# Optimization experiments

Measured on AMD Instinct MI355X. Metric: run time of the kernel, lower is better.

## Reference

```python
import jax, jax.numpy as jnp
import numpy as np

B, LQ, LK, E, H, NF, NE, HID = 4, 8192, 8192, 256, 8, 2, 4, 256


def _split(x, h):
    b, l, e = x.shape
    return x.reshape(b, l, h, e // h).transpose(0, 2, 1, 3)  # (B,H,L,D)


def _merge(x):
    b, h, l, d = x.shape
    return x.transpose(0, 2, 1, 3).reshape(b, l, h * d)


def _experts(x, W1, b1, W2, b2, W3, b3):
    # x: (B,N,in); W*: (E, out, in). Returns (E,B,N,out). Exact (erf) GELU as torch.
    h = jax.nn.gelu(jnp.einsum('bni,ehi->ebnh', x, W1) + b1[:, None, None, :], approximate=False)
    h = jax.nn.gelu(jnp.einsum('ebnh,egh->ebng', h, W2) + b2[:, None, None, :], approximate=False)
    return jnp.einsum('ebng,eog->ebno', h, W3) + b3[:, None, None, :]


def _combine(expert_out, scores):
    # expert_out: (E,B,N,out); scores: (B,N,1,E) -> (B,N,out)
    return jnp.einsum('ebno,bne->bno', expert_out, scores[:, :, 0, :])


def _forward(scores, query, input_functions,
             ca_Wq, ca_bq, ca_Wk, ca_bk, ca_Wv, ca_bv, ca_Wo, ca_bo,
             sa_Wq, sa_bq, sa_Wk, sa_bk, sa_Wv, sa_bv, sa_Wo, sa_bo,
             f1_W1, f1_b1, f1_W2, f1_b2, f1_W3, f1_b3,
             f2_W1, f2_b1, f2_W2, f2_b2, f2_W3, f2_b3):
    h = H
    # ---- cross attention over NF input functions ----
    q = jax.nn.softmax(_split(query @ ca_Wq.T + ca_bq, h), -1)  # (B,H,Lq,D)
    k = jnp.einsum('fble,fde->fbld', input_functions, ca_Wk) + ca_bk[:, None, None, :]
    v = jnp.einsum('fble,fde->fbld', input_functions, ca_Wv) + ca_bv[:, None, None, :]
    f, b, lk, e = k.shape
    d = e // h
    k = jax.nn.softmax(k.reshape(f, b, lk, h, d).transpose(0, 1, 3, 2, 4), -1)  # (F,B,H,Lk,D)
    v = v.reshape(f, b, lk, h, d).transpose(0, 1, 3, 2, 4)
    k_sum = k.sum(3, keepdims=True)                       # (F,B,H,1,D)
    alpha = 1.0 / (q[None] * k_sum).sum(-1, keepdims=True)  # (F,B,H,Lq,1)
    tmp = jnp.einsum('fbhld,fbhlv->fbhdv', k, v)          # (F,B,H,D,D)
    out = (alpha * jnp.einsum('bhld,fbhdv->fbhlv', q, tmp)).mean(0)  # (B,H,Lq,D)
    ca = (_merge(q) + _merge(out)) @ ca_Wo.T + ca_bo
    # expert FFN1 + score-weighted combine, residual
    query = query + _combine(_experts(ca, f1_W1, f1_b1, f1_W2, f1_b2, f1_W3, f1_b3), scores)
    # ---- self attention ----
    q2 = jax.nn.softmax(_split(query @ sa_Wq.T + sa_bq, h), -1)
    k2 = jax.nn.softmax(_split(query @ sa_Wk.T + sa_bk, h), -1)
    v2 = _split(query @ sa_Wv.T + sa_bv, h)
    k_sum2 = k2.sum(2, keepdims=True)
    alpha2 = 1.0 / (q2 * k_sum2).sum(-1, keepdims=True)
    tmp2 = jnp.einsum('bhld,bhlv->bhdv', k2, v2)
    out2 = alpha2 * jnp.einsum('bhld,bhdv->bhlv', q2, tmp2)
    sa = (_merge(q2) + _merge(out2)) @ sa_Wo.T + sa_bo
    query = query + _combine(_experts(sa, f2_W1, f2_b1, f2_W2, f2_b2, f2_W3, f2_b3), scores)
    return query


def setup_inputs() -> dict:
    ks = iter(jax.random.split(jax.random.key(0), 64))
    def p(shape):
        return jax.random.normal(next(ks), shape, jnp.float32) * 0.02
    inp = {
        'scores': jax.random.uniform(next(ks), (B, LQ, 1, NE), jnp.float32),
        'query': jax.random.normal(next(ks), (B, LQ, E), jnp.float32),
        'input_functions': jax.random.normal(next(ks), (NF, B, LK, E), jnp.float32),
        'ca_Wq': p((E, E)), 'ca_bq': p((E,)),
        'ca_Wk': p((NF, E, E)), 'ca_bk': p((NF, E)),
        'ca_Wv': p((NF, E, E)), 'ca_bv': p((NF, E)),
        'ca_Wo': p((E, E)), 'ca_bo': p((E,)),
        'sa_Wq': p((E, E)), 'sa_bq': p((E,)),
        'sa_Wk': p((E, E)), 'sa_bk': p((E,)),
        'sa_Wv': p((E, E)), 'sa_bv': p((E,)),
        'sa_Wo': p((E, E)), 'sa_bo': p((E,)),
        'f1_W1': p((NE, HID, E)), 'f1_b1': p((NE, HID)),
        'f1_W2': p((NE, HID, HID)), 'f1_b2': p((NE, HID)),
        'f1_W3': p((NE, HID, HID)), 'f1_b3': p((NE, HID)),
        'f2_W1': p((NE, HID, E)), 'f2_b1': p((NE, HID)),
        'f2_W2': p((NE, HID, HID)), 'f2_b2': p((NE, HID)),
        'f2_W3': p((NE, HID, HID)), 'f2_b3': p((NE, HID)),
    }
    return inp


def reference(scores, query, input_functions,
              ca_Wq, ca_bq, ca_Wk, ca_bk, ca_Wv, ca_bv, ca_Wo, ca_bo,
              sa_Wq, sa_bq, sa_Wk, sa_bk, sa_Wv, sa_bv, sa_Wo, sa_bo,
              f1_W1, f1_b1, f1_W2, f1_b2, f1_W3, f1_b3,
              f2_W1, f2_b1, f2_W2, f2_b2, f2_W3, f2_b3):
    return _forward(scores, query, input_functions,
                    ca_Wq, ca_bq, ca_Wk, ca_bk, ca_Wv, ca_bv, ca_Wo, ca_bo,
                    sa_Wq, sa_bq, sa_Wk, sa_bk, sa_Wv, sa_bv, sa_Wo, sa_bo,
                    f1_W1, f1_b1, f1_W2, f1_b2, f1_W3, f1_b3,
                    f2_W1, f2_b1, f2_W2, f2_b2, f2_W3, f2_b3)
```

## Files before the change

### kernel.cpp

```cpp
#include <hip/hip_runtime.h>


typedef unsigned short u16;
typedef __attribute__((ext_vector_type(8))) short   bs8;
typedef __attribute__((ext_vector_type(4))) float   f32x4;
typedef __attribute__((ext_vector_type(16))) float  f32x16;

__device__ __forceinline__ float bf2f(u16 u) {
  union { float f; unsigned i; } c; c.i = ((unsigned)u) << 16; return c.f;
}
__device__ __forceinline__ u16 f2bf(float f) {
  union { float f; unsigned i; } c; c.f = f;
  unsigned x = c.i;
  return (u16)((x + 0x7fffu + ((x >> 16) & 1u)) >> 16);
}
__device__ __forceinline__ unsigned pack2(float a, float b) {
  return (unsigned)f2bf(a) | ((unsigned)f2bf(b) << 16);
}
__device__ __forceinline__ float gelu_f(float x) {
  const float t = x * (0.7978845608f + 0.0356774081f * x * x);
  return x * __builtin_amdgcn_rcpf(1.f + __expf(-2.f * t));
}

#define EPI_PLAIN 0
#define EPI_QSM   4

template <bool AF32, int EPI>
__global__ __launch_bounds__(256, 4) void gemm256(
    const void* __restrict__ Ain, const u16* __restrict__ W,
    const float* __restrict__ bias, u16* __restrict__ outb) {
  __shared__ int4 ash[512];
  __shared__ int4 wsh[1024];
  const int tid = threadIdx.x;
  const int m0 = blockIdx.x * 64, n0 = blockIdx.y * 128;
  const int wave = tid >> 6, lane = tid & 63;
  const int wm = (wave >> 1) * 32, wn = (wave & 1) * 64;
  const int lr = lane & 15, lk = lane >> 4;
  f32x4 acc[2][4];
#pragma unroll
  for (int m = 0; m < 2; ++m)
#pragma unroll
    for (int n = 0; n < 4; ++n) acc[m][n] = f32x4{0.f, 0.f, 0.f, 0.f};

  const float* Af = (const float*)Ain;
  const u16*   Ab = (const u16*)Ain;

  for (int kt = 0; kt < 4; ++kt) {
    const int k0 = kt * 64;
    if (kt) __syncthreads();
#pragma unroll
    for (int it = 0; it < 2; ++it) {
      const int s = tid + it * 256;
      const int row = s >> 3, c16 = s & 7;
      const int dst = (row << 3) | (c16 ^ (row & 7));
      const long src = (long)(m0 + row) * 256 + k0 + c16 * 8;
      int4 val;
      if constexpr (AF32) {
        const float4* p = (const float4*)(Af + src);
        const float4 x = p[0], y = p[1];
        val.x = pack2(x.x, x.y); val.y = pack2(x.z, x.w);
        val.z = pack2(y.x, y.y); val.w = pack2(y.z, y.w);
      } else {
        val = *(const int4*)(Ab + src);
      }
      ash[dst] = val;
    }
#pragma unroll
    for (int it = 0; it < 4; ++it) {
      const int s = tid + it * 256;
      const int row = s >> 3, c16 = s & 7;
      const int dst = (row << 3) | (c16 ^ (row & 7));
      wsh[dst] = *(const int4*)(W + (long)(n0 + row) * 256 + k0 + c16 * 8);
    }
    __syncthreads();
#pragma unroll
    for (int kk = 0; kk < 2; ++kk) {
      bs8 af[2], wf[4];
#pragma unroll
      for (int m = 0; m < 2; ++m) {
        const int row = wm + m * 16 + lr;
        af[m] = *(const bs8*)&ash[(row << 3) | ((kk * 4 + lk) ^ (row & 7))];
      }
#pragma unroll
      for (int n = 0; n < 4; ++n) {
        const int row = wn + n * 16 + lr;
        wf[n] = *(const bs8*)&wsh[(row << 3) | ((kk * 4 + lk) ^ (row & 7))];
      }
#pragma unroll
      for (int m = 0; m < 2; ++m)
#pragma unroll
        for (int n = 0; n < 4; ++n)
          acc[m][n] = __builtin_amdgcn_mfma_f32_16x16x32_bf16(af[m], wf[n],
                                                              acc[m][n], 0, 0, 0);
    }
  }
  if constexpr (EPI == EPI_QSM) {
#pragma unroll
    for (int m = 0; m < 2; ++m) {
      const int rb = m0 + wm + m * 16 + lk * 4;
#pragma unroll
      for (int j = 0; j < 4; ++j) {
#pragma unroll
        for (int hh = 0; hh < 2; ++hh) {
          const int c0 = n0 + wn + (2 * hh) * 16 + lr;
          const float p0 = __expf(acc[m][2 * hh][j] + bias[c0]);
          const float p1 = __expf(acc[m][2 * hh + 1][j] + bias[c0 + 16]);
          float s = p0 + p1;
#pragma unroll
          for (int o = 8; o >= 1; o >>= 1) s += __shfl_xor(s, o);
          const float inv = 1.0f / s;
          outb[(long)(rb + j) * 256 + c0]      = f2bf(p0 * inv);
          outb[(long)(rb + j) * 256 + c0 + 16] = f2bf(p1 * inv);
        }
      }
    }
  } else {
#pragma unroll
    for (int m = 0; m < 2; ++m) {
      const int rb = m0 + wm + m * 16 + lk * 4;
#pragma unroll
      for (int n = 0; n < 4; ++n) {
        const int gc = n0 + wn + n * 16 + lr;
        const float bv = bias[gc];
#pragma unroll
        for (int j = 0; j < 4; ++j)
          outb[(long)(rb + j) * 256 + gc] = f2bf(acc[m][n][j] + bv);
      }
    }
  }
}

__global__ __launch_bounds__(1024, 4) void ffn4(
    const u16* __restrict__ X, const u16* __restrict__ WX, int wbase,
    const float* __restrict__ b1, const float* __restrict__ b2,
    const float* __restrict__ b3, const float* __restrict__ scores,
    const float* __restrict__ csrc, float* __restrict__ outf) {
  __shared__ int4 xsh[2048];
  __shared__ int4 hsh[2048];
  const int tid = threadIdx.x, wave = tid >> 6, lane = tid & 63;
  const int wm = (wave >> 3) * 32;
  const int wn8 = wave & 7;
  const int lr = lane & 15, lk = lane >> 4;
  const long m0 = (long)blockIdx.x * 64;

#pragma unroll
  for (int it = 0; it < 2; ++it) {
    const int s = tid + it * 1024;
    const int row = s >> 5, c8 = s & 31;
    const int cs = (c8 & 24) | ((c8 ^ row) & 7);
    xsh[row * 32 + cs] = *(const int4*)(X + (m0 + row) * 256 + c8 * 8);
  }
  __syncthreads();

  f32x4 oacc[2][2];
#pragma unroll
  for (int m = 0; m < 2; ++m)
#pragma unroll
    for (int n = 0; n < 2; ++n) oacc[m][n] = f32x4{0.f, 0.f, 0.f, 0.f};
  f32x4 acc[2][2];

  for (int e = 0; e < 4; ++e) {
#pragma unroll 1
    for (int l = 0; l < 3; ++l) {
      const u16* wp = WX + (long)(wbase + l * 4 + e) * 65536 + (long)lane * 8;
      const int4* asrc = (l == 0) ? xsh : hsh;
#pragma unroll
      for (int m = 0; m < 2; ++m)
#pragma unroll
        for (int n = 0; n < 2; ++n) acc[m][n] = f32x4{0.f, 0.f, 0.f, 0.f};
#pragma unroll
      for (int kt = 0; kt < 8; ++kt) {
        bs8 af[2], wf[2];
        const int c8 = kt * 4 + lk;
#pragma unroll
        for (int m = 0; m < 2; ++m) {
          const int row = wm + m * 16 + lr;
          const int cs = (c8 & 24) | ((c8 ^ row) & 7);
          af[m] = *(const bs8*)&asrc[row * 32 + cs];
        }
#pragma unroll
        for (int n = 0; n < 2; ++n)
          wf[n] = *(const bs8*)(wp + ((kt * 16 + wn8 * 2 + n) << 9));
        __builtin_amdgcn_s_setprio(1);
#pragma unroll
        for (int m = 0; m < 2; ++m)
#pragma unroll
          for (int n = 0; n < 2; ++n)
            acc[m][n] = __builtin_amdgcn_mfma_f32_16x16x32_bf16(
                af[m], wf[n], acc[m][n], 0, 0, 0);
        __builtin_amdgcn_s_setprio(0);
      }
      if (l < 2) {
        __syncthreads();
        const float* bb = (l == 0 ? b1 : b2) + e * 256;
        u16* hp = (u16*)hsh;
#pragma unroll
        for (int m = 0; m < 2; ++m)
#pragma unroll
          for (int n = 0; n < 2; ++n) {
            const int col = wn8 * 32 + n * 16 + lr;
            const float bv = bb[col];
            const int c8w = col >> 3;
#pragma unroll
            for (int j = 0; j < 4; ++j) {
              const int row = wm + m * 16 + lk * 4 + j;
              const int cs = (c8w & 24) | ((c8w ^ row) & 7);
              hp[row * 256 + cs * 8 + (col & 7)] =
                  f2bf(gelu_f(acc[m][n][j] + bv));
            }
          }
        __syncthreads();
      } else {
#pragma unroll
        for (int m = 0; m < 2; ++m) {
#pragma unroll
          for (int j = 0; j < 4; ++j) {
            const float sc = scores[(m0 + wm + m * 16 + lk * 4 + j) * 4 + e];
#pragma unroll
            for (int n = 0; n < 2; ++n)
              oacc[m][n][j] +=
                  sc * (acc[m][n][j] + b3[e * 256 + wn8 * 32 + n * 16 + lr]);
          }
        }
      }
    }
  }
#pragma unroll
  for (int m = 0; m < 2; ++m) {
#pragma unroll
    for (int n = 0; n < 2; ++n) {
      const int col = wn8 * 32 + n * 16 + lr;
#pragma unroll
      for (int j = 0; j < 4; ++j) {
        const long idx = (m0 + wm + m * 16 + lk * 4 + j) * 256 + col;
        outf[idx] = csrc[idx] + oacc[m][n][j];
      }
    }
  }
}

__global__ __launch_bounds__(1024, 4) void kvstats(
    const float* __restrict__ A0, const float* __restrict__ A1,
    const u16* __restrict__ Wk0, const u16* __restrict__ Wk1,
    const u16* __restrict__ Wv0, const u16* __restrict__ Wv1,
    const float* __restrict__ bk0, const float* __restrict__ bk1,
    const float* __restrict__ bv0, const float* __restrict__ bv1,
    float* __restrict__ pks, float* __restrict__ ptm) {
  __shared__ __align__(16) char smem[73728];
  int4* ash  = (int4*)smem;
  int4* wksh = ash + 512;
  int4* wvsh = wksh + 2048;
  u16* KnT = (u16*)smem;
  u16* VT  = KnT + 256 * 72;
  const int tid = threadIdx.x;
  const int wave = tid >> 6, lane = tid & 63;
  const int lr = lane & 15, lk = lane >> 4;
  const int kvsel = wave >> 3, w3 = wave & 7;
  const int wm = (w3 >> 2) * 32, wn = (w3 & 3) * 64;
  const int fb = blockIdx.y, ch = blockIdx.x;
  const int f = fb >> 2, b = fb & 3;
  const float* Ain = f ? A1 : A0;
  const u16* Wk = f ? Wk1 : Wk0;
  const u16* Wv = f ? Wv1 : Wv0;
  const float* bk = f ? bk1 : bk0;
  const float* bv = f ? bv1 : bv0;
  const long r0 = (long)b * 8192 + (long)ch * 64;

  f32x4 acc[2][4];
#pragma unroll
  for (int m = 0; m < 2; ++m)
#pragma unroll
    for (int n = 0; n < 4; ++n) acc[m][n] = f32x4{0.f, 0.f, 0.f, 0.f};

  for (int kt = 0; kt < 4; ++kt) {
    const int k0 = kt * 64;
    if (kt) __syncthreads();
    if (tid < 512) {
      const int row = tid >> 3, c16 = tid & 7;
      const int dst = (row << 3) | (c16 ^ (row & 7));
      const float4* p = (const float4*)(Ain + (r0 + row) * 256 + k0 + c16 * 8);
      const float4 x = p[0], y = p[1];
      int4 val;
      val.x = pack2(x.x, x.y); val.y = pack2(x.z, x.w);
      val.z = pack2(y.x, y.y); val.w = pack2(y.z, y.w);
      ash[dst] = val;
    }
#pragma unroll
    for (int it = 0; it < 2; ++it) {
      const int s = tid + it * 1024;
      const int row = s >> 3, c16 = s & 7;
      const int dst = (row << 3) | (c16 ^ (row & 7));
      wksh[dst] = *(const int4*)(Wk + (long)row * 256 + k0 + c16 * 8);
      wvsh[dst] = *(const int4*)(Wv + (long)row * 256 + k0 + c16 * 8);
    }
    __syncthreads();
    const int4* wsh = kvsel ? wvsh : wksh;
#pragma unroll
    for (int kk = 0; kk < 2; ++kk) {
      bs8 af[2], wf[4];
#pragma unroll
      for (int m = 0; m < 2; ++m) {
        const int row = wm + m * 16 + lr;
        af[m] = *(const bs8*)&ash[(row << 3) | ((kk * 4 + lk) ^ (row & 7))];
      }
#pragma unroll
      for (int n = 0; n < 4; ++n) {
        const int row = wn + n * 16 + lr;
        wf[n] = *(const bs8*)&wsh[(row << 3) | ((kk * 4 + lk) ^ (row & 7))];
      }
#pragma unroll
      for (int m = 0; m < 2; ++m)
#pragma unroll
        for (int n = 0; n < 4; ++n)
          acc[m][n] = __builtin_amdgcn_mfma_f32_16x16x32_bf16(af[m], wf[n],
                                                              acc[m][n], 0, 0, 0);
    }
  }
  __syncthreads();

  const float* bias = kvsel ? bv : bk;
  if (kvsel == 0) {
#pragma unroll
    for (int m = 0; m < 2; ++m)
#pragma unroll
      for (int j = 0; j < 4; ++j)
#pragma unroll
        for (int hh = 0; hh < 2; ++hh) {
          const int c0 = wn + (2 * hh) * 16 + lr;
          const float p0 = __expf(acc[m][2 * hh][j] + bias[c0]);
          const float p1 = __expf(acc[m][2 * hh + 1][j] + bias[c0 + 16]);
          float s = p0 + p1;
#pragma unroll
          for (int o = 8; o >= 1; o >>= 1) s += __shfl_xor(s, o);
          const float inv = 1.0f / s;
          acc[m][2 * hh][j] = p0 * inv;
          acc[m][2 * hh + 1][j] = p1 * inv;
        }
  }
  {
    u16* T = kvsel ? VT : KnT;
#pragma unroll
    for (int m = 0; m < 2; ++m) {
      const int rb = wm + m * 16 + lk * 4;
#pragma unroll
      for (int n = 0; n < 4; ++n) {
        const int col = wn + n * 16 + lr;
        float v0 = acc[m][n][0], v1 = acc[m][n][1];
        float v2 = acc[m][n][2], v3 = acc[m][n][3];
        if (kvsel) {
          const float bb = bias[col];
          v0 += bb; v1 += bb; v2 += bb; v3 += bb;
        }
        uint2 w;
        w.x = pack2(v0, v1); w.y = pack2(v2, v3);
        *(uint2*)(T + col * 72 + rb) = w;
      }
    }
  }
  __syncthreads();

  if (kvsel == 0) {
    const int h = w3;
    f32x16 aT, aK;
#pragma unroll
    for (int r = 0; r < 16; ++r) { aT[r] = 0.f; aK[r] = 0.f; }
    bs8 ones;
#pragma unroll
    for (int e = 0; e < 8; ++e) ones[e] = (short)0x3F80;
    const u16* kcol = KnT + (h * 32 + (lane & 31)) * 72;
    const u16* vcol = VT  + (h * 32 + (lane & 31)) * 72;
    const int hi8 = (lane >> 5) * 8;
#pragma unroll
    for (int ks = 0; ks < 4; ++ks) {
      const bs8 a  = *(const bs8*)(kcol + ks * 16 + hi8);
      const bs8 vb = *(const bs8*)(vcol + ks * 16 + hi8);
      aT = __builtin_amdgcn_mfma_f32_32x32x16_bf16(vb, a, aT, 0, 0, 0);
      aK = __builtin_amdgcn_mfma_f32_32x32x16_bf16(a, ones, aK, 0, 0, 0);
    }
    const long blk = (long)fb * gridDim.x + ch;
    float* po = ptm + blk * 8192 + h * 1024;
#pragma unroll
    for (int r = 0; r < 16; ++r) {
      const int dv = (r & 3) + 8 * (r >> 2) + 4 * (lane >> 5);
      po[dv * 32 + (lane & 31)] = aT[r];
    }
    if ((lane & 31) == 0) {
#pragma unroll
      for (int r = 0; r < 16; ++r) {
        const int dk = (r & 3) + 8 * (r >> 2) + 4 * (lane >> 5);
        pks[blk * 256 + h * 32 + dk] = aK[r];
      }
    }
  }
}

__global__ void reduceStats(const float* __restrict__ pk,
                            const float* __restrict__ pt,
                            float* __restrict__ ksum, float* __restrict__ tmp) {
  const int b = blockIdx.y;
  const int i = blockIdx.x * 256 + threadIdx.x;
  float s = 0.f;
  if (i < 256) {
    const float* p = pk + (long)b * 128 * 256 + i;
    for (int c = 0; c < 128; ++c) s += p[c * 256];
    ksum[(long)b * 256 + i] = s;
  } else {
    const int j = i - 256;
    const float* p = pt + (long)b * 128 * 8192 + j;
    for (int c = 0; c < 128; ++c) s += p[c * 8192];
    tmp[(long)b * 8192 + j] = s;
  }
}

template <int F>
__global__ __launch_bounds__(256, 2) void mixk(const u16* __restrict__ q,
                                               const float* __restrict__ ksum,
                                               const float* __restrict__ tmp,
                                               u16* __restrict__ out) {
  constexpr int LF = (F == 2) ? 1 : 0;
  constexpr int QS = 264;
  __shared__ u16 qsh[64 * QS];
  __shared__ float alsh[64][17];
  __shared__ float ksh[8][F * 36];
  const int t = threadIdx.x;
  const int h = t >> 5, dv = t & 31;
  const int b = blockIdx.y;
  const long row0 = (long)b * 8192 + (long)blockIdx.x * 64;

#pragma unroll
  for (int it = 0; it < 8; ++it) {
    const int i = t + it * 256;
    const int r = i >> 5, c = i & 31;
    *(int4*)&qsh[r * QS + c * 8] = *(const int4*)&q[(row0 + r) * 256 + c * 8];
  }
#pragma unroll
  for (int f = 0; f < F; ++f)
    ksh[h][f * 36 + dv] = ksum[((long)f * 4 + b) * 256 + t];
  float tr[F][32];
#pragma unroll
  for (int f = 0; f < F; ++f) {
    const float* tp = tmp + ((long)f * 4 + b) * 8192 + h * 1024 + dv * 32;
#pragma unroll
    for (int c = 0; c < 8; ++c) {
      const float4 v = *(const float4*)(tp + c * 4);
      tr[f][c * 4] = v.x; tr[f][c * 4 + 1] = v.y;
      tr[f][c * 4 + 2] = v.z; tr[f][c * 4 + 3] = v.w;
    }
  }
  __syncthreads();

  for (int d = t; d < 64 * 8 * F; d += 256) {
    const int f = d & (F - 1);
    const int hh = (d >> LF) & 7;
    const int r = d >> (3 + LF);
    const u16* qp = &qsh[r * QS + hh * 32];
    const float* kp = &ksh[hh][f * 36];
    float s = 0.f;
#pragma unroll
    for (int c = 0; c < 4; ++c) {
      const bs8 qa = *(const bs8*)(qp + c * 8);
#pragma unroll
      for (int j = 0; j < 8; ++j) s += bf2f((u16)qa[j]) * kp[c * 8 + j];
    }
    alsh[r][(hh << LF) | f] = 1.0f / s;
  }
  __syncthreads();

#pragma unroll 2
  for (int r = 0; r < 64; ++r) {
    float qr[32];
    const u16* qp = &qsh[r * QS + h * 32];
#pragma unroll
    for (int c = 0; c < 4; ++c) {
      const bs8 qa = *(const bs8*)(qp + c * 8);
#pragma unroll
      for (int j = 0; j < 8; ++j) qr[c * 8 + j] = bf2f((u16)qa[j]);
    }
    float acc = 0.f;
#pragma unroll
    for (int f = 0; f < F; ++f) {
      float s0 = 0.f, s1 = 0.f;
#pragma unroll
      for (int dk = 0; dk < 32; dk += 2) {
        s0 += qr[dk] * tr[f][dk];
        s1 += qr[dk + 1] * tr[f][dk + 1];
      }
      acc += (s0 + s1) * alsh[r][(h << LF) | f];
    }
    const float qv = bf2f(qsh[r * QS + t]);
    out[(row0 + r) * 256 + t] = f2bf(qv + acc * (1.0f / (float)F));
  }
}

struct WTab10 { const float* p[10]; };
__global__ void convW(WTab10 tab, u16* __restrict__ dst) {
  const int s = blockIdx.y;
  const long i = ((long)blockIdx.x * 256 + threadIdx.x) * 4;
  const float4 v = *(const float4*)(tab.p[s] + i);
  ushort4 o;
  o.x = f2bf(v.x); o.y = f2bf(v.y); o.z = f2bf(v.z); o.w = f2bf(v.w);
  *(ushort4*)(dst + (long)s * 65536 + i) = o;
}

struct WTab24 { const float* p[24]; };
__global__ void convWX(WTab24 tab, u16* __restrict__ dst) {
  const int s = blockIdx.y;
  const int o8 = blockIdx.x * 256 + threadIdx.x;
  const int kt = o8 >> 10, nt = (o8 >> 6) & 15, lane = o8 & 63;
  const int row = nt * 16 + (lane & 15);
  const int col = kt * 32 + (lane >> 4) * 8;
  const float* src = tab.p[s] + row * 256 + col;
  const float4 a = *(const float4*)src;
  const float4 b = *(const float4*)(src + 4);
  int4 val;
  val.x = pack2(a.x, a.y); val.y = pack2(a.z, a.w);
  val.z = pack2(b.x, b.y); val.w = pack2(b.z, b.w);
  *(int4*)(dst + (long)s * 65536 + (long)o8 * 8) = val;
}

extern "C" void kernel_launch(void* const* d_in, const int* in_sizes, int n_in,
                              void* d_out, int out_size, void* d_ws, size_t ws_size,
                              hipStream_t stream) {
  (void)in_sizes; (void)n_in; (void)out_size; (void)ws_size;
  const float* scores = (const float*)d_in[0];
  const float* query  = (const float*)d_in[1];
  const float* IF     = (const float*)d_in[2];
  const float* ca_Wq = (const float*)d_in[3];  const float* ca_bq = (const float*)d_in[4];
  const float* ca_Wk = (const float*)d_in[5];  const float* ca_bk = (const float*)d_in[6];
  const float* ca_Wv = (const float*)d_in[7];  const float* ca_bv = (const float*)d_in[8];
  const float* ca_Wo = (const float*)d_in[9];  const float* ca_bo = (const float*)d_in[10];
  const float* sa_Wq = (const float*)d_in[11]; const float* sa_bq = (const float*)d_in[12];
  const float* sa_Wk = (const float*)d_in[13]; const float* sa_bk = (const float*)d_in[14];
  const float* sa_Wv = (const float*)d_in[15]; const float* sa_bv = (const float*)d_in[16];
  const float* sa_Wo = (const float*)d_in[17]; const float* sa_bo = (const float*)d_in[18];
  const float* f1W1 = (const float*)d_in[19]; const float* f1b1 = (const float*)d_in[20];
  const float* f1W2 = (const float*)d_in[21]; const float* f1b2 = (const float*)d_in[22];
  const float* f1W3 = (const float*)d_in[23]; const float* f1b3 = (const float*)d_in[24];
  const float* f2W1 = (const float*)d_in[25]; const float* f2b1 = (const float*)d_in[26];
  const float* f2W2 = (const float*)d_in[27]; const float* f2b2 = (const float*)d_in[28];
  const float* f2W3 = (const float*)d_in[29]; const float* f2b3 = (const float*)d_in[30];

  char* ws = (char*)d_ws;
  u16* X0 = (u16*)(ws);
  u16* X1 = (u16*)(ws + 16777216);
  u16* X2 = (u16*)(ws + 33554432);
  float* ptmBig = (float*)(ws + 16777216);
  u16* W16 = (u16*)(ws + 67108864);
  u16* WX  = (u16*)(ws + 68419584);
  float* ksum = (float*)(ws + 71565312);
  float* tmpb = (float*)(ws + 71573504);
  float* pks  = (float*)(ws + 71835648);
  float* qacc = (float*)d_out;

  WTab10 tab;
  tab.p[0] = ca_Wq; tab.p[1] = ca_Wk; tab.p[2] = ca_Wk + 65536;
  tab.p[3] = ca_Wv; tab.p[4] = ca_Wv + 65536; tab.p[5] = ca_Wo;
  tab.p[6] = sa_Wq; tab.p[7] = sa_Wk; tab.p[8] = sa_Wv; tab.p[9] = sa_Wo;
  convW<<<dim3(64, 10), 256, 0, stream>>>(tab, W16);

  WTab24 tabx;
  for (int e = 0; e < 4; ++e) {
    tabx.p[0 + e]  = f1W1 + e * 65536;
    tabx.p[4 + e]  = f1W2 + e * 65536;
    tabx.p[8 + e]  = f1W3 + e * 65536;
    tabx.p[12 + e] = f2W1 + e * 65536;
    tabx.p[16 + e] = f2W2 + e * 65536;
    tabx.p[20 + e] = f2W3 + e * 65536;
  }
  convWX<<<dim3(32, 24), 256, 0, stream>>>(tabx, WX);

  const dim3 gg(512, 2), gb(256);
  gemm256<true, EPI_QSM><<<gg, gb, 0, stream>>>(query, W16 + 0 * 65536L, ca_bq, X0);
  kvstats<<<dim3(128, 8), 1024, 0, stream>>>(
      IF, IF + 8388608L,
      W16 + 1 * 65536L, W16 + 2 * 65536L, W16 + 3 * 65536L, W16 + 4 * 65536L,
      ca_bk, ca_bk + 256, ca_bv, ca_bv + 256, pks, ptmBig);
  reduceStats<<<dim3(33, 8), 256, 0, stream>>>(pks, ptmBig, ksum, tmpb);
  mixk<2><<<dim3(128, 4), 256, 0, stream>>>(X0, ksum, tmpb, X1);
  gemm256<false, EPI_PLAIN><<<gg, gb, 0, stream>>>(X1, W16 + 5 * 65536L, ca_bo, X2);
  ffn4<<<512, 1024, 0, stream>>>(X2, WX, 0, f1b1, f1b2, f1b3, scores, query, qacc);
  gemm256<true, EPI_QSM><<<gg, gb, 0, stream>>>(qacc, W16 + 6 * 65536L, sa_bq, X0);
  kvstats<<<dim3(128, 4), 1024, 0, stream>>>(
      qacc, qacc,
      W16 + 7 * 65536L, W16 + 7 * 65536L, W16 + 8 * 65536L, W16 + 8 * 65536L,
      sa_bk, sa_bk, sa_bv, sa_bv, pks, ptmBig);
  reduceStats<<<dim3(33, 4), 256, 0, stream>>>(pks, ptmBig, ksum, tmpb);
  mixk<1><<<dim3(128, 4), 256, 0, stream>>>(X0, ksum, tmpb, X1);
  gemm256<false, EPI_PLAIN><<<gg, gb, 0, stream>>>(X1, W16 + 9 * 65536L, sa_bo, X2);
  ffn4<<<512, 1024, 0, stream>>>(X2, WX, 12, f2b1, f2b2, f2b3, scores, qacc, qacc);
}
```

Baseline: 415.1 us.

## Fuse output projection into expert FFN kernel and repartition waves by column

The attention output projection (Wo GEMM plus bias) now runs inside ffn4 as a prologue, so the separate gemm256 launch and the X2 round trip through global memory are dropped. ffn4's wave layout changes from a 2x8 grid of 32x32 tiles to 16 waves that each own a 16-column strip across all 64 rows. Each weight fragment is loaded once per k-step and reused by four MFMAs, and the next fragment is prefetched in software. The weight repack layout is reordered to match, with two extra slots for the Wo matrices, and the workspace offsets shift accordingly. In exchange, each block does an extra 256x256 GEMM, and A-fragment LDS reads per wave double.

```diff
diff --git a/kernel.cpp b/kernel.cpp
--- a/kernel.cpp
+++ b/kernel.cpp
@@ -131,16 +131,17 @@
 }
 
 __global__ __launch_bounds__(1024, 4) void ffn4(
-    const u16* __restrict__ X, const u16* __restrict__ WX, int wbase,
+    const u16* __restrict__ Xin, const u16* __restrict__ WX,
+    int wPslot, int wbase, const float* __restrict__ bP,
     const float* __restrict__ b1, const float* __restrict__ b2,
     const float* __restrict__ b3, const float* __restrict__ scores,
     const float* __restrict__ csrc, float* __restrict__ outf) {
   __shared__ int4 xsh[2048];
   __shared__ int4 hsh[2048];
   const int tid = threadIdx.x, wave = tid >> 6, lane = tid & 63;
-  const int wm = (wave >> 3) * 32;
-  const int wn8 = wave & 7;
+  const int ng = wave;
   const int lr = lane & 15, lk = lane >> 4;
+  const int col = ng * 16 + lr;
   const long m0 = (long)blockIdx.x * 64;
 
 #pragma unroll
@@ -148,93 +149,119 @@
     const int s = tid + it * 1024;
     const int row = s >> 5, c8 = s & 31;
     const int cs = (c8 & 24) | ((c8 ^ row) & 7);
-    xsh[row * 32 + cs] = *(const int4*)(X + (m0 + row) * 256 + c8 * 8);
+    hsh[row * 32 + cs] = *(const int4*)(Xin + (m0 + row) * 256 + c8 * 8);
   }
   __syncthreads();
 
-  f32x4 oacc[2][2];
-#pragma unroll
-  for (int m = 0; m < 2; ++m)
-#pragma unroll
-    for (int n = 0; n < 2; ++n) oacc[m][n] = f32x4{0.f, 0.f, 0.f, 0.f};
-  f32x4 acc[2][2];
+  f32x4 acc[4];
+
+  {
+    const u16* wp = WX + (((long)wPslot) << 16) + (ng << 12) + lane * 8;
+#pragma unroll
+    for (int m = 0; m < 4; ++m) acc[m] = f32x4{0.f, 0.f, 0.f, 0.f};
+    bs8 wf, wfn;
+    wf = *(const bs8*)(wp);
+#pragma unroll
+    for (int kt = 0; kt < 8; ++kt) {
+      if (kt < 7) wfn = *(const bs8*)(wp + (kt + 1) * 512);
+      bs8 af[4];
+      const int c8 = kt * 4 + lk;
+#pragma unroll
+      for (int m = 0; m < 4; ++m) {
+        const int row = m * 16 + lr;
+        const int cs = (c8 & 24) | ((c8 ^ row) & 7);
+        af[m] = *(const bs8*)&hsh[row * 32 + cs];
+      }
+      __builtin_amdgcn_s_setprio(1);
+#pragma unroll
+      for (int m = 0; m < 4; ++m)
+        acc[m] = __builtin_amdgcn_mfma_f32_16x16x32_bf16(af[m], wf, acc[m],
+                                                         0, 0, 0);
+      __builtin_amdgcn_s_setprio(0);
+      wf = wfn;
+    }
+    __syncthreads();
+    const float bv = bP[col];
+    u16* xp = (u16*)xsh;
+    const int c8w = col >> 3;
+#pragma unroll
+    for (int m = 0; m < 4; ++m)
+#pragma unroll
+      for (int j = 0; j < 4; ++j) {
+        const int row = m * 16 + lk * 4 + j;
+        const int cs = (c8w & 24) | ((c8w ^ row) & 7);
+        xp[row * 256 + cs * 8 + (col & 7)] = f2bf(acc[m][j] + bv);
+      }
+    __syncthreads();
+  }
+
+  f32x4 oacc[4];
+#pragma unroll
+  for (int m = 0; m < 4; ++m) oacc[m] = f32x4{0.f, 0.f, 0.f, 0.f};
 
   for (int e = 0; e < 4; ++e) {
 #pragma unroll 1
     for (int l = 0; l < 3; ++l) {
-      const u16* wp = WX + (long)(wbase + l * 4 + e) * 65536 + (long)lane * 8;
+      const u16* wp = WX + (((long)(wbase + l * 4 + e)) << 16) +
+                      (ng << 12) + lane * 8;
       const int4* asrc = (l == 0) ? xsh : hsh;
 #pragma unroll
-      for (int m = 0; m < 2; ++m)
-#pragma unroll
-        for (int n = 0; n < 2; ++n) acc[m][n] = f32x4{0.f, 0.f, 0.f, 0.f};
+      for (int m = 0; m < 4; ++m) acc[m] = f32x4{0.f, 0.f, 0.f, 0.f};
+      bs8 wf, wfn;
+      wf = *(const bs8*)(wp);
 #pragma unroll
       for (int kt = 0; kt < 8; ++kt) {
-        bs8 af[2], wf[2];
+        if (kt < 7) wfn = *(const bs8*)(wp + (kt + 1) * 512);
+        bs8 af[4];
         const int c8 = kt * 4 + lk;
 #pragma unroll
-        for (int m = 0; m < 2; ++m) {
-          const int row = wm + m * 16 + lr;
+        for (int m = 0; m < 4; ++m) {
+          const int row = m * 16 + lr;
           const int cs = (c8 & 24) | ((c8 ^ row) & 7);
           af[m] = *(const bs8*)&asrc[row * 32 + cs];
         }
-#pragma unroll
-        for (int n = 0; n < 2; ++n)
-          wf[n] = *(const bs8*)(wp + ((kt * 16 + wn8 * 2 + n) << 9));
         __builtin_amdgcn_s_setprio(1);
 #pragma unroll
-        for (int m = 0; m < 2; ++m)
-#pragma unroll
-          for (int n = 0; n < 2; ++n)
-            acc[m][n] = __builtin_amdgcn_mfma_f32_16x16x32_bf16(
-                af[m], wf[n], acc[m][n], 0, 0, 0);
+        for (int m = 0; m < 4; ++m)
+          acc[m] = __builtin_amdgcn_mfma_f32_16x16x32_bf16(af[m], wf, acc[m],
+                                                           0, 0, 0);
         __builtin_amdgcn_s_setprio(0);
+        wf = wfn;
       }
       if (l < 2) {
         __syncthreads();
-        const float* bb = (l == 0 ? b1 : b2) + e * 256;
+        const float bv = (l == 0 ? b1 : b2)[e * 256 + col];
         u16* hp = (u16*)hsh;
-#pragma unroll
-        for (int m = 0; m < 2; ++m)
-#pragma unroll
-          for (int n = 0; n < 2; ++n) {
-            const int col = wn8 * 32 + n * 16 + lr;
-            const float bv = bb[col];
-            const int c8w = col >> 3;
-#pragma unroll
-            for (int j = 0; j < 4; ++j) {
-              const int row = wm + m * 16 + lk * 4 + j;
-              const int cs = (c8w & 24) | ((c8w ^ row) & 7);
-              hp[row * 256 + cs * 8 + (col & 7)] =
-                  f2bf(gelu_f(acc[m][n][j] + bv));
-            }
+        const int c8w = col >> 3;
+#pragma unroll
+        for (int m = 0; m < 4; ++m)
+#pragma unroll
+          for (int j = 0; j < 4; ++j) {
+            const int row = m * 16 + lk * 4 + j;
+            const int cs = (c8w & 24) | ((c8w ^ row) & 7);
+            hp[row * 256 + cs * 8 + (col & 7)] =
+                f2bf(gelu_f(acc[m][j] + bv));
           }
         __syncthreads();
       } else {
-#pragma unroll
-        for (int m = 0; m < 2; ++m) {
+        const float b3v = b3[e * 256 + col];
+#pragma unroll
+        for (int m = 0; m < 4; ++m) {
 #pragma unroll
           for (int j = 0; j < 4; ++j) {
-            const float sc = scores[(m0 + wm + m * 16 + lk * 4 + j) * 4 + e];
-#pragma unroll
-            for (int n = 0; n < 2; ++n)
-              oacc[m][n][j] +=
-                  sc * (acc[m][n][j] + b3[e * 256 + wn8 * 32 + n * 16 + lr]);
+            const float sc = scores[(m0 + m * 16 + lk * 4 + j) * 4 + e];
+            oacc[m][j] += sc * (acc[m][j] + b3v);
           }
         }
       }
     }
   }
 #pragma unroll
-  for (int m = 0; m < 2; ++m) {
-#pragma unroll
-    for (int n = 0; n < 2; ++n) {
-      const int col = wn8 * 32 + n * 16 + lr;
-#pragma unroll
-      for (int j = 0; j < 4; ++j) {
-        const long idx = (m0 + wm + m * 16 + lk * 4 + j) * 256 + col;
-        outf[idx] = csrc[idx] + oacc[m][n][j];
-      }
+  for (int m = 0; m < 4; ++m) {
+#pragma unroll
+    for (int j = 0; j < 4; ++j) {
+      const long idx = (m0 + m * 16 + lk * 4 + j) * 256 + col;
+      outf[idx] = csrc[idx] + oacc[m][j];
     }
   }
 }
@@ -502,12 +529,14 @@
   *(ushort4*)(dst + (long)s * 65536 + i) = o;
 }
 
-struct WTab24 { const float* p[24]; };
-__global__ void convWX(WTab24 tab, u16* __restrict__ dst) {
+struct WTab26 { const float* p[26]; };
+__global__ void convWX(WTab26 tab, u16* __restrict__ dst) {
   const int s = blockIdx.y;
   const int o8 = blockIdx.x * 256 + threadIdx.x;
-  const int kt = o8 >> 10, nt = (o8 >> 6) & 15, lane = o8 & 63;
-  const int row = nt * 16 + (lane & 15);
+  const int lane = o8 & 63;
+  const int kt = (o8 >> 6) & 7;
+  const int ng = o8 >> 9;
+  const int row = ng * 16 + (lane & 15);
   const int col = kt * 32 + (lane >> 4) * 8;
   const float* src = tab.p[s] + row * 256 + col;
   const float4 a = *(const float4*)src;
@@ -543,13 +572,12 @@
   char* ws = (char*)d_ws;
   u16* X0 = (u16*)(ws);
   u16* X1 = (u16*)(ws + 16777216);
-  u16* X2 = (u16*)(ws + 33554432);
   float* ptmBig = (float*)(ws + 16777216);
   u16* W16 = (u16*)(ws + 67108864);
   u16* WX  = (u16*)(ws + 68419584);
-  float* ksum = (float*)(ws + 71565312);
-  float* tmpb = (float*)(ws + 71573504);
-  float* pks  = (float*)(ws + 71835648);
+  float* ksum = (float*)(ws + 71827456);
+  float* tmpb = (float*)(ws + 71835648);
+  float* pks  = (float*)(ws + 72097792);
   float* qacc = (float*)d_out;
 
   WTab10 tab;
@@ -558,7 +586,7 @@
   tab.p[6] = sa_Wq; tab.p[7] = sa_Wk; tab.p[8] = sa_Wv; tab.p[9] = sa_Wo;
   convW<<<dim3(64, 10), 256, 0, stream>>>(tab, W16);
 
-  WTab24 tabx;
+  WTab26 tabx;
   for (int e = 0; e < 4; ++e) {
     tabx.p[0 + e]  = f1W1 + e * 65536;
     tabx.p[4 + e]  = f1W2 + e * 65536;
@@ -567,7 +595,9 @@
     tabx.p[16 + e] = f2W2 + e * 65536;
     tabx.p[20 + e] = f2W3 + e * 65536;
   }
-  convWX<<<dim3(32, 24), 256, 0, stream>>>(tabx, WX);
+  tabx.p[24] = ca_Wo;
+  tabx.p[25] = sa_Wo;
+  convWX<<<dim3(32, 26), 256, 0, stream>>>(tabx, WX);
 
   const dim3 gg(512, 2), gb(256);
   gemm256<true, EPI_QSM><<<gg, gb, 0, stream>>>(query, W16 + 0 * 65536L, ca_bq, X0);
@@ -577,8 +607,8 @@
       ca_bk, ca_bk + 256, ca_bv, ca_bv + 256, pks, ptmBig);
   reduceStats<<<dim3(33, 8), 256, 0, stream>>>(pks, ptmBig, ksum, tmpb);
   mixk<2><<<dim3(128, 4), 256, 0, stream>>>(X0, ksum, tmpb, X1);
-  gemm256<false, EPI_PLAIN><<<gg, gb, 0, stream>>>(X1, W16 + 5 * 65536L, ca_bo, X2);
-  ffn4<<<512, 1024, 0, stream>>>(X2, WX, 0, f1b1, f1b2, f1b3, scores, query, qacc);
+  ffn4<<<512, 1024, 0, stream>>>(X1, WX, 24, 0, ca_bo,
+                                 f1b1, f1b2, f1b3, scores, query, qacc);
   gemm256<true, EPI_QSM><<<gg, gb, 0, stream>>>(qacc, W16 + 6 * 65536L, sa_bq, X0);
   kvstats<<<dim3(128, 4), 1024, 0, stream>>>(
       qacc, qacc,
@@ -586,6 +616,6 @@
       sa_bk, sa_bk, sa_bv, sa_bv, pks, ptmBig);
   reduceStats<<<dim3(33, 4), 256, 0, stream>>>(pks, ptmBig, ksum, tmpb);
   mixk<1><<<dim3(128, 4), 256, 0, stream>>>(X0, ksum, tmpb, X1);
-  gemm256<false, EPI_PLAIN><<<gg, gb, 0, stream>>>(X1, W16 + 9 * 65536L, sa_bo, X2);
-  ffn4<<<512, 1024, 0, stream>>>(X2, WX, 12, f2b1, f2b2, f2b3, scores, qacc, qacc);
-}
+  ffn4<<<512, 1024, 0, stream>>>(X1, WX, 25, 12, sa_bo,
+                                 f2b1, f2b2, f2b3, scores, qacc, qacc);
+}
```

Measured after the change: 429.7 us. +3.5%, slower.
